# Kernel optimization log

Hardware: AMD Instinct MI355X
Metric: run time of the kernel (lower is better)

## Reference

```python
import jax, jax.numpy as jnp
import numpy as np

B, T, C, H = 32, 2048, 1024, 64


def setup_inputs() -> dict:
    key = jax.random.key(0)
    k1, k2, k3, k4 = jax.random.split(key, 4)
    x = jax.random.normal(k1, (B, T, C), dtype=jnp.float32)
    # nn.Linear(C, H, bias=False) weights, stored here as [C, H] for x @ W
    s = 1.0 / np.sqrt(C)
    Wk = jax.random.uniform(k2, (C, H), jnp.float32, -s, s)
    Wq = jax.random.uniform(k3, (C, H), jnp.float32, -s, s)
    Wv = jax.random.uniform(k4, (C, H), jnp.float32, -s, s)
    return {"x": x, "Wk": Wk, "Wq": Wq, "Wv": Wv}


def reference(x, Wk, Wq, Wv):
    # projections: [B,T,C] @ [C,H] -> [B,T,H]
    k = jnp.einsum('btc,ch->bth', x, Wk)
    q = jnp.einsum('btc,ch->bth', x, Wq)
    v = jnp.einsum('btc,ch->bth', x, Wv)
    Hd = k.shape[-1]
    # attention scores [B,T,T], scaled by head_size^-0.5
    scores = jnp.einsum('bqh,bkh->bqk', q, k) * (Hd ** -0.5)
    # causal mask: masked_fill where triu(ones, 1)==1 -> -inf (mask strict upper triangle)
    Tq = x.shape[1]
    causal = jnp.tril(jnp.ones((Tq, Tq), dtype=bool))  # True = keep
    scores = jnp.where(causal, scores, -jnp.inf)
    attn = jax.nn.softmax(scores, axis=-1)
    # dropout: identity in eval/reference mode
    out = jnp.einsum('bqk,bkh->bqh', attn, v)
    return out
```

## Files before the change

kernel.cpp:

```cpp
#include <hip/hip_runtime.h>
#include <hip/hip_bf16.h>

typedef short bf16x8 __attribute__((ext_vector_type(8)));
typedef float f32x4 __attribute__((ext_vector_type(4)));

#define B_ 32
#define T_ 2048
#define C_ 1024
#define H_ 64

__device__ __forceinline__ ushort f2bf(float f) {
  union { float f; unsigned u; } v; v.f = f;
  unsigned u = v.u;
  return (ushort)((u + 0x7FFFu + ((u >> 16) & 1u)) >> 16);
}

__device__ __forceinline__ bf16x8 pack8(float4 a, float4 b) {
  union { __hip_bfloat162 h; short2 s; } t;
  bf16x8 r;
  t.h = __float22bfloat162_rn(make_float2(a.x, a.y)); r[0] = t.s.x; r[1] = t.s.y;
  t.h = __float22bfloat162_rn(make_float2(a.z, a.w)); r[2] = t.s.x; r[3] = t.s.y;
  t.h = __float22bfloat162_rn(make_float2(b.x, b.y)); r[4] = t.s.x; r[5] = t.s.y;
  t.h = __float22bfloat162_rn(make_float2(b.z, b.w)); r[6] = t.s.x; r[7] = t.s.y;
  return r;
}

__device__ __forceinline__ void async_copy16(void* lds, const void* g) {
  __builtin_amdgcn_global_load_lds(
      (const __attribute__((address_space(1))) unsigned int*)g,
      (__attribute__((address_space(3))) unsigned int*)lds, 16, 0, 0);
}

__global__ __launch_bounds__(256) void wconv_kernel(
    const float* __restrict__ Wk, const float* __restrict__ Wq,
    const float* __restrict__ Wv, ushort* __restrict__ Wt) {
  int idx = blockIdx.x * 256 + threadIdx.x;
  if (idx >= 3 * 64 * C_) return;
  int n = idx >> 10, c = idx & 1023;
  int mat = n >> 6, h = n & 63;
  const float* W = (mat == 0) ? Wk : (mat == 1 ? Wq : Wv);
  float v = W[c * 64 + h];
  if (mat == 1) v *= 0.18033688011112042f;
  Wt[idx] = f2bf(v);
}

__global__ __launch_bounds__(256, 4) void qkv_kernel(
    const float* __restrict__ x, const ushort* __restrict__ Wt,
    ushort* __restrict__ Kb, ushort* __restrict__ Qb, ushort* __restrict__ Vt) {
  __shared__ __align__(16) ushort Bs[192 * 64];
  int tid = threadIdx.x;
  int wave = tid >> 6, lane = tid & 63, quad = lane >> 4, l16 = lane & 15;
  int r0 = blockIdx.x * 64;
  const float* xr = x + (size_t)(r0 + wave * 16 + l16) * C_;

  f32x4 acc[12];
#pragma unroll
  for (int nt = 0; nt < 12; ++nt) acc[nt] = (f32x4){0.f, 0.f, 0.f, 0.f};

  for (int k0 = 0; k0 < C_; k0 += 64) {
    __syncthreads();
#pragma unroll
    for (int i = 0; i < 6; ++i) {
      int id = tid + 256 * i;
      int n = id >> 3, p = id & 7, c = p ^ (n & 7);
      async_copy16((char*)Bs + id * 16, Wt + (size_t)n * C_ + k0 + c * 8);
    }
    float4 a0 = *(const float4*)(xr + k0 + quad * 8);
    float4 a1 = *(const float4*)(xr + k0 + quad * 8 + 4);
    float4 a2 = *(const float4*)(xr + k0 + 32 + quad * 8);
    float4 a3 = *(const float4*)(xr + k0 + 32 + quad * 8 + 4);
    __syncthreads();

    bf16x8 af0 = pack8(a0, a1);
    bf16x8 af1 = pack8(a2, a3);
#pragma unroll
    for (int nt = 0; nt < 12; ++nt) {
      int n = nt * 16 + l16;
      bf16x8 b0 = *(const bf16x8*)(Bs + n * 64 + ((quad ^ (l16 & 7)) << 3));
      bf16x8 b1 = *(const bf16x8*)(Bs + n * 64 + (((4 + quad) ^ (l16 & 7)) << 3));
      acc[nt] = __builtin_amdgcn_mfma_f32_16x16x32_bf16(af0, b0, acc[nt], 0, 0, 0);
      acc[nt] = __builtin_amdgcn_mfma_f32_16x16x32_bf16(af1, b1, acc[nt], 0, 0, 0);
    }
  }

  int b = r0 >> 11;
  int rowbase = r0 + wave * 16 + quad * 4;
#pragma unroll
  for (int nt = 0; nt < 12; ++nt) {
    int mat = nt >> 2;
    int h = (nt & 3) * 16 + l16;
    if (mat == 2) {
      ushort4 pv;
      pv.x = f2bf(acc[nt][0]); pv.y = f2bf(acc[nt][1]);
      pv.z = f2bf(acc[nt][2]); pv.w = f2bf(acc[nt][3]);
      *(ushort4*)(&Vt[(size_t)b * H_ * T_ + (size_t)h * T_ + (rowbase & (T_ - 1))]) = pv;
    } else {
      ushort* dst = (mat == 0) ? Kb : Qb;
#pragma unroll
      for (int r = 0; r < 4; ++r)
        dst[(size_t)(rowbase + r) * H_ + h] = f2bf(acc[nt][r]);
    }
  }
}

__global__ __launch_bounds__(256, 2) void attn_kernel(
    const ushort* __restrict__ Qb, const ushort* __restrict__ Kb,
    const ushort* __restrict__ Vt, float* __restrict__ out) {
  __shared__ __align__(16) ushort Ks[2][64 * 64];
  __shared__ __align__(16) ushort Vs[2][64 * 64];
  __shared__ __align__(16) ushort Pl[4 * 16 * 80];

  int tid = threadIdx.x;
  int wave = tid >> 6, lane = tid & 63, quad = lane >> 4, l16 = lane & 15;
  int bid = blockIdx.x;
  int xcd = bid & 7, wi = bid >> 3;
  int batch = xcd * 4 + (wi & 3);
  int spair = wi >> 2;
  const ushort* Qbase = Qb + (size_t)batch * T_ * H_;
  const ushort* Kbase = Kb + (size_t)batch * T_ * H_;
  const ushort* Vbase = Vt + (size_t)batch * H_ * T_;
  ushort* Pw = Pl + wave * 16 * 80;

  auto stage = [&](int jb, int buf) {
    int j0 = jb * 64;
#pragma unroll
    for (int g = 0; g < 2; ++g) {
      int id = tid + 256 * g;
      int r = id >> 3, p = id & 7, c = p ^ (r & 7);
      async_copy16((char*)&Ks[buf][0] + id * 16,
                   Kbase + (size_t)(j0 + r) * H_ + c * 8);
      async_copy16((char*)&Vs[buf][0] + id * 16,
                   Vbase + (size_t)r * T_ + j0 + c * 8);
    }
  };

#pragma unroll 1
  for (int half = 0; half < 2; ++half) {
    int qseg = half ? spair : 31 - spair;
    int q0 = qseg * 64 + wave * 16;
    const ushort* qr = Qbase + (size_t)(q0 + l16) * H_;
    bf16x8 qf0 = *(const bf16x8*)(qr + quad * 8);
    bf16x8 qf1 = *(const bf16x8*)(qr + 32 + quad * 8);

    f32x4 o[4];
    float m_i[4], l_i[4];
#pragma unroll
    for (int i = 0; i < 4; ++i) {
      o[i] = (f32x4){0.f, 0.f, 0.f, 0.f};
      m_i[i] = -1e30f; l_i[i] = 0.f;
    }

    int jb_last = qseg;
    __syncthreads();
    stage(0, 0);
    int cur = 0;
    for (int jb = 0; jb <= jb_last; ++jb, cur ^= 1) {
      int j0 = jb * 64;
      __syncthreads();
      if (jb < jb_last) stage(jb + 1, cur ^ 1);
      const ushort* KsC = &Ks[cur][0];
      const ushort* VsC = &Vs[cur][0];

      f32x4 sv[4];
#pragma unroll
      for (int nt = 0; nt < 4; ++nt) {
        int n = nt * 16 + l16;
        bf16x8 kf0 = *(const bf16x8*)(KsC + n * 64 + ((quad ^ (l16 & 7)) << 3));
        bf16x8 kf1 = *(const bf16x8*)(KsC + n * 64 + (((4 + quad) ^ (l16 & 7)) << 3));
        f32x4 z = (f32x4){0.f, 0.f, 0.f, 0.f};
        z = __builtin_amdgcn_mfma_f32_16x16x32_bf16(qf0, kf0, z, 0, 0, 0);
        z = __builtin_amdgcn_mfma_f32_16x16x32_bf16(qf1, kf1, z, 0, 0, 0);
        sv[nt] = z;
      }

      if (jb == jb_last) {
        int rowg = q0 + quad * 4;
#pragma unroll
        for (int nt = 0; nt < 4; ++nt) {
          int col = j0 + nt * 16 + l16;
#pragma unroll
          for (int rr = 0; rr < 4; ++rr)
            if (col > rowg + rr) sv[nt][rr] = -1e30f;
        }
      }

      float pm[4];
#pragma unroll
      for (int rr = 0; rr < 4; ++rr) {
        float v = fmaxf(fmaxf(sv[0][rr], sv[1][rr]), fmaxf(sv[2][rr], sv[3][rr]));
        v = fmaxf(v, __shfl_xor(v, 1));
        v = fmaxf(v, __shfl_xor(v, 2));
        v = fmaxf(v, __shfl_xor(v, 4));
        v = fmaxf(v, __shfl_xor(v, 8));
        pm[rr] = v;
      }
      bool grow = (pm[0] > m_i[0] + 8.f) || (pm[1] > m_i[1] + 8.f) ||
                  (pm[2] > m_i[2] + 8.f) || (pm[3] > m_i[3] + 8.f);
      if (__any(grow)) {
#pragma unroll
        for (int rr = 0; rr < 4; ++rr) {
          float mn = fmaxf(m_i[rr], pm[rr]);
          float alpha = exp2f(m_i[rr] - mn);
          m_i[rr] = mn;
          l_i[rr] *= alpha;
#pragma unroll
          for (int ht = 0; ht < 4; ++ht) o[ht][rr] *= alpha;
        }
      }

      float rsum[4] = {0.f, 0.f, 0.f, 0.f};
#pragma unroll
      for (int nt = 0; nt < 4; ++nt)
#pragma unroll
        for (int rr = 0; rr < 4; ++rr) {
          float p = exp2f(sv[nt][rr] - m_i[rr]);
          rsum[rr] += p;
          Pw[(quad * 4 + rr) * 80 + nt * 16 + l16] = f2bf(p);
        }
#pragma unroll
      for (int rr = 0; rr < 4; ++rr) l_i[rr] += rsum[rr];

      bf16x8 pf0 = *(const bf16x8*)(&Pw[l16 * 80 + quad * 8]);
      bf16x8 pf1 = *(const bf16x8*)(&Pw[l16 * 80 + 32 + quad * 8]);
#pragma unroll
      for (int ht = 0; ht < 4; ++ht) {
        int hrow = ht * 16 + l16;
        bf16x8 vf0 = *(const bf16x8*)(VsC + hrow * 64 + ((quad ^ (l16 & 7)) << 3));
        bf16x8 vf1 = *(const bf16x8*)(VsC + hrow * 64 + (((4 + quad) ^ (l16 & 7)) << 3));
        o[ht] = __builtin_amdgcn_mfma_f32_16x16x32_bf16(pf0, vf0, o[ht], 0, 0, 0);
        o[ht] = __builtin_amdgcn_mfma_f32_16x16x32_bf16(pf1, vf1, o[ht], 0, 0, 0);
      }
    }

#pragma unroll
    for (int rr = 0; rr < 4; ++rr) {
      float v = l_i[rr];
      v += __shfl_xor(v, 1);
      v += __shfl_xor(v, 2);
      v += __shfl_xor(v, 4);
      v += __shfl_xor(v, 8);
      l_i[rr] = __builtin_amdgcn_rcpf(v);
    }
    int rowbase = q0 + quad * 4;
#pragma unroll
    for (int ht = 0; ht < 4; ++ht)
#pragma unroll
      for (int rr = 0; rr < 4; ++rr)
        out[((size_t)batch * T_ + rowbase + rr) * H_ + ht * 16 + l16] =
            o[ht][rr] * l_i[rr];
  }
}

extern "C" void kernel_launch(void* const* d_in, const int* in_sizes, int n_in,
                              void* d_out, int out_size, void* d_ws, size_t ws_size,
                              hipStream_t stream) {
  const float* x  = (const float*)d_in[0];
  const float* Wk = (const float*)d_in[1];
  const float* Wq = (const float*)d_in[2];
  const float* Wv = (const float*)d_in[3];
  float* out = (float*)d_out;

  ushort* Wt = (ushort*)d_ws;
  ushort* Kb = (ushort*)((char*)d_ws + (1 << 19));
  ushort* Qb = Kb + (size_t)B_ * T_ * H_;
  ushort* Vt = Qb + (size_t)B_ * T_ * H_;

  hipLaunchKernelGGL(wconv_kernel, dim3(768), dim3(256), 0, stream, Wk, Wq, Wv, Wt);
  hipLaunchKernelGGL(qkv_kernel, dim3(1024), dim3(256), 0, stream, x, Wt, Kb, Qb, Vt);
  hipLaunchKernelGGL(attn_kernel, dim3(512), dim3(256), 0, stream, Qb, Kb, Vt, out);
}
```

Before: 442.1 us.

## Widen attention KV tile to 128 with swizzled P buffer and MFMA priority

Each loop iteration now processes 128 keys instead of 64. The K and V staging buffers grow to 128 columns, and the V shared-memory copy uses a 16-way XOR swizzle. This halves the number of barrier and softmax-rescale steps per query segment. The P scratch buffer gets an XOR-swizzled 128-wide layout to avoid bank conflicts, and the MFMA sections are bracketed with s_setprio to favour matrix issue. In exchange, up to 64 keys of the final chunk are fully masked but still computed, register pressure is higher, and LDS use rises to about 80KB per block, which may limit occupancy.

```diff
diff --git a/kernel.cpp b/kernel.cpp
--- a/kernel.cpp
+++ b/kernel.cpp
@@ -106,9 +106,9 @@
 __global__ __launch_bounds__(256, 2) void attn_kernel(
     const ushort* __restrict__ Qb, const ushort* __restrict__ Kb,
     const ushort* __restrict__ Vt, float* __restrict__ out) {
-  __shared__ __align__(16) ushort Ks[2][64 * 64];
-  __shared__ __align__(16) ushort Vs[2][64 * 64];
-  __shared__ __align__(16) ushort Pl[4 * 16 * 80];
+  __shared__ __align__(16) ushort Ks[2][128 * 64];
+  __shared__ __align__(16) ushort Vs[2][64 * 128];
+  __shared__ __align__(16) ushort Pl[4][16 * 128];
 
   int tid = threadIdx.x;
   int wave = tid >> 6, lane = tid & 63, quad = lane >> 4, l16 = lane & 15;
@@ -119,16 +119,21 @@
   const ushort* Qbase = Qb + (size_t)batch * T_ * H_;
   const ushort* Kbase = Kb + (size_t)batch * T_ * H_;
   const ushort* Vbase = Vt + (size_t)batch * H_ * T_;
-  ushort* Pw = Pl + wave * 16 * 80;
-
-  auto stage = [&](int jb, int buf) {
-    int j0 = jb * 64;
-#pragma unroll
-    for (int g = 0; g < 2; ++g) {
+  ushort* Pw = &Pl[wave][0];
+
+  auto stage = [&](int jc, int buf) {
+    int j0 = jc * 128;
+#pragma unroll
+    for (int g = 0; g < 4; ++g) {
       int id = tid + 256 * g;
-      int r = id >> 3, p = id & 7, c = p ^ (r & 7);
+      int n = id >> 3, p = id & 7, c = p ^ (n & 7);
       async_copy16((char*)&Ks[buf][0] + id * 16,
-                   Kbase + (size_t)(j0 + r) * H_ + c * 8);
+                   Kbase + (size_t)(j0 + n) * H_ + c * 8);
+    }
+#pragma unroll
+    for (int g = 0; g < 4; ++g) {
+      int id = tid + 256 * g;
+      int r = id >> 4, p = id & 15, c = p ^ (r & 15);
       async_copy16((char*)&Vs[buf][0] + id * 16,
                    Vbase + (size_t)r * T_ + j0 + c * 8);
     }
@@ -150,20 +155,22 @@
       m_i[i] = -1e30f; l_i[i] = 0.f;
     }
 
-    int jb_last = qseg;
+    int nch = (qseg >> 1) + 1;
     __syncthreads();
     stage(0, 0);
     int cur = 0;
-    for (int jb = 0; jb <= jb_last; ++jb, cur ^= 1) {
-      int j0 = jb * 64;
+#pragma unroll 1
+    for (int jc = 0; jc < nch; ++jc, cur ^= 1) {
+      int j0 = jc * 128;
       __syncthreads();
-      if (jb < jb_last) stage(jb + 1, cur ^ 1);
+      if (jc + 1 < nch) stage(jc + 1, cur ^ 1);
       const ushort* KsC = &Ks[cur][0];
       const ushort* VsC = &Vs[cur][0];
 
-      f32x4 sv[4];
-#pragma unroll
-      for (int nt = 0; nt < 4; ++nt) {
+      f32x4 sv[8];
+      __builtin_amdgcn_s_setprio(1);
+#pragma unroll
+      for (int nt = 0; nt < 8; ++nt) {
         int n = nt * 16 + l16;
         bf16x8 kf0 = *(const bf16x8*)(KsC + n * 64 + ((quad ^ (l16 & 7)) << 3));
         bf16x8 kf1 = *(const bf16x8*)(KsC + n * 64 + (((4 + quad) ^ (l16 & 7)) << 3));
@@ -172,11 +179,12 @@
         z = __builtin_amdgcn_mfma_f32_16x16x32_bf16(qf1, kf1, z, 0, 0, 0);
         sv[nt] = z;
       }
-
-      if (jb == jb_last) {
+      __builtin_amdgcn_s_setprio(0);
+
+      if (jc == nch - 1) {
         int rowg = q0 + quad * 4;
 #pragma unroll
-        for (int nt = 0; nt < 4; ++nt) {
+        for (int nt = 0; nt < 8; ++nt) {
           int col = j0 + nt * 16 + l16;
 #pragma unroll
           for (int rr = 0; rr < 4; ++rr)
@@ -187,7 +195,8 @@
       float pm[4];
 #pragma unroll
       for (int rr = 0; rr < 4; ++rr) {
-        float v = fmaxf(fmaxf(sv[0][rr], sv[1][rr]), fmaxf(sv[2][rr], sv[3][rr]));
+        float v = fmaxf(fmaxf(fmaxf(sv[0][rr], sv[1][rr]), fmaxf(sv[2][rr], sv[3][rr])),
+                        fmaxf(fmaxf(sv[4][rr], sv[5][rr]), fmaxf(sv[6][rr], sv[7][rr])));
         v = fmaxf(v, __shfl_xor(v, 1));
         v = fmaxf(v, __shfl_xor(v, 2));
         v = fmaxf(v, __shfl_xor(v, 4));
@@ -210,26 +219,33 @@
 
       float rsum[4] = {0.f, 0.f, 0.f, 0.f};
 #pragma unroll
-      for (int nt = 0; nt < 4; ++nt)
+      for (int nt = 0; nt < 8; ++nt)
 #pragma unroll
         for (int rr = 0; rr < 4; ++rr) {
           float p = exp2f(sv[nt][rr] - m_i[rr]);
           rsum[rr] += p;
-          Pw[(quad * 4 + rr) * 80 + nt * 16 + l16] = f2bf(p);
+          int row = quad * 4 + rr;
+          int swz = (nt * 2 + (l16 >> 3)) ^ row;
+          Pw[row * 128 + (swz << 3) + (l16 & 7)] = f2bf(p);
         }
 #pragma unroll
       for (int rr = 0; rr < 4; ++rr) l_i[rr] += rsum[rr];
 
-      bf16x8 pf0 = *(const bf16x8*)(&Pw[l16 * 80 + quad * 8]);
-      bf16x8 pf1 = *(const bf16x8*)(&Pw[l16 * 80 + 32 + quad * 8]);
+      bf16x8 pf[4];
+#pragma unroll
+      for (int k = 0; k < 4; ++k)
+        pf[k] = *(const bf16x8*)(&Pw[l16 * 128 + (((quad + 4 * k) ^ l16) << 3)]);
+      __builtin_amdgcn_s_setprio(1);
 #pragma unroll
       for (int ht = 0; ht < 4; ++ht) {
         int hrow = ht * 16 + l16;
-        bf16x8 vf0 = *(const bf16x8*)(VsC + hrow * 64 + ((quad ^ (l16 & 7)) << 3));
-        bf16x8 vf1 = *(const bf16x8*)(VsC + hrow * 64 + (((4 + quad) ^ (l16 & 7)) << 3));
-        o[ht] = __builtin_amdgcn_mfma_f32_16x16x32_bf16(pf0, vf0, o[ht], 0, 0, 0);
-        o[ht] = __builtin_amdgcn_mfma_f32_16x16x32_bf16(pf1, vf1, o[ht], 0, 0, 0);
-      }
+#pragma unroll
+        for (int k = 0; k < 4; ++k) {
+          bf16x8 vf = *(const bf16x8*)(VsC + hrow * 128 + (((4 * k + quad) ^ l16) << 3));
+          o[ht] = __builtin_amdgcn_mfma_f32_16x16x32_bf16(pf[k], vf, o[ht], 0, 0, 0);
+        }
+      }
+      __builtin_amdgcn_s_setprio(0);
     }
 
 #pragma unroll
```

Result: no change. 435.2 us (-1.6%).
